# Optimization experiments

Hardware: AMD Instinct MI355X
Metric: run time of the kernel (lower is better)

## Reference

```python
import jax, jax.numpy as jnp
import numpy as np

N = 20000   # genes
E = 160000  # directed edges (self-loops added in forward, as PyG GATv2Conv does by default)
D = 64      # input feature dim
H1, C1 = 8, 128  # conv1 heads / channels
LRELU_SLOPE = 0.2
LN_EPS = 1e-5


def setup_inputs() -> dict:
    key = jax.random.key(0)
    ks = jax.random.split(key, 20)
    s = 0.05
    inp = {
        "x": jax.random.normal(ks[0], (N, D), dtype=jnp.float32),
        "edge_index": jax.random.randint(ks[1], (2, E), 0, N, dtype=jnp.int64),
        # conv1 (GATv2Conv D -> H1*C1, concat)
        "Wl1": jax.random.normal(ks[2], (D, H1 * C1), dtype=jnp.float32) * s,
        "bl1": jax.random.normal(ks[3], (H1 * C1,), dtype=jnp.float32) * s,
        "Wr1": jax.random.normal(ks[4], (D, H1 * C1), dtype=jnp.float32) * s,
        "br1": jax.random.normal(ks[5], (H1 * C1,), dtype=jnp.float32) * s,
        "att1": jax.random.normal(ks[6], (H1, C1), dtype=jnp.float32) * s,
        "b1": jax.random.normal(ks[7], (H1 * C1,), dtype=jnp.float32) * s,
        # skip Linear(D -> H1*C1)
        "Wskip": jax.random.normal(ks[8], (D, H1 * C1), dtype=jnp.float32) * s,
        "bskip": jax.random.normal(ks[9], (H1 * C1,), dtype=jnp.float32) * s,
        # LayerNorm(H1*C1)
        "g1": jnp.ones((H1 * C1,), dtype=jnp.float32),
        "beta1": jnp.zeros((H1 * C1,), dtype=jnp.float32),
        # conv2 (GATv2Conv H1*C1 -> 2, heads=1, concat=False)
        "Wl2": jax.random.normal(ks[10], (H1 * C1, 2), dtype=jnp.float32) * s,
        "bl2": jax.random.normal(ks[11], (2,), dtype=jnp.float32) * s,
        "Wr2": jax.random.normal(ks[12], (H1 * C1, 2), dtype=jnp.float32) * s,
        "br2": jax.random.normal(ks[13], (2,), dtype=jnp.float32) * s,
        "att2": jax.random.normal(ks[14], (1, 2), dtype=jnp.float32) * s,
        "b2": jax.random.normal(ks[15], (2,), dtype=jnp.float32) * s,
    }
    return inp


def _gatv2(x, src, dst, Wl, bl, Wr, br, att, bias, heads, ch, concat):
    """PyG GATv2Conv (eval mode): message src -> dst, scatter-softmax over dst."""
    n = x.shape[0]
    xl = (x @ Wl + bl).reshape(n, heads, ch)  # source-side transform
    xr = (x @ Wr + br).reshape(n, heads, ch)  # target-side transform
    e = jax.nn.leaky_relu(xl[src] + xr[dst], LRELU_SLOPE)   # [E,H,C]
    alpha = jnp.einsum('ehc,hc->eh', e, att)                 # [E,H]
    amax = jax.ops.segment_max(alpha, dst, num_segments=n)   # [N,H]
    ex = jnp.exp(alpha - amax[dst])
    denom = jax.ops.segment_sum(ex, dst, num_segments=n)
    alpha = ex / (denom[dst] + 1e-16)
    msg = xl[src] * alpha[..., None]                          # [E,H,C]
    out = jax.ops.segment_sum(msg, dst, num_segments=n)      # [N,H,C]
    out = out.reshape(n, heads * ch) if concat else out.mean(axis=1)
    return out + bias


def _layernorm(x, g, b):
    mu = x.mean(axis=-1, keepdims=True)
    var = ((x - mu) ** 2).mean(axis=-1, keepdims=True)
    return (x - mu) * jax.lax.rsqrt(var + LN_EPS) * g + b


def reference(x, edge_index, Wl1, bl1, Wr1, br1, att1, b1, Wskip, bskip,
              g1, beta1, Wl2, bl2, Wr2, br2, att2, b2):
    n = x.shape[0]
    loop = jnp.arange(n, dtype=edge_index.dtype)  # add_self_loops=True (PyG default)
    src = jnp.concatenate([edge_index[0], loop])
    dst = jnp.concatenate([edge_index[1], loop])
    x1 = _gatv2(x, src, dst, Wl1, bl1, Wr1, br1, att1, b1, H1, C1, True) + (x @ Wskip + bskip)
    x1 = jax.nn.elu(_layernorm(x1, g1, beta1))
    # dropout is a no-op in eval mode
    return _gatv2(x1, src, dst, Wl2, bl2, Wr2, br2, att2, b2, 1, 2, False)
```

## Files before the change

kernel.cpp:

```cpp
#include <hip/hip_runtime.h>
#include <hip/hip_bf16.h>
#include <hip/hip_fp16.h>
#include <math.h>

static constexpr int D  = 64;
static constexpr int F1 = 1024;
static constexpr int NTOT = 3072;
static constexpr int EW  = 64;

typedef _Float16 f16x8 __attribute__((ext_vector_type(8)));
typedef _Float16 h2    __attribute__((ext_vector_type(2)));
typedef float    f32x4 __attribute__((ext_vector_type(4)));
typedef unsigned int u32x4 __attribute__((ext_vector_type(4)));

__device__ __forceinline__ float lrelu(float x) { return x > 0.f ? x : 0.2f * x; }

__device__ __forceinline__ float dot2f(h2 a, h2 b, float c) {
#if __has_builtin(__builtin_amdgcn_fdot2)
    return __builtin_amdgcn_fdot2(a, b, c, false);
#else
    return c + (float)a[0] * (float)b[0] + (float)a[1] * (float)b[1];
#endif
}

__device__ __forceinline__ float red16(float p) {
    int v = __builtin_bit_cast(int, p);
    p += __builtin_bit_cast(float, __builtin_amdgcn_mov_dpp(v, 0xB1, 0xF, 0xF, true));
    v = __builtin_bit_cast(int, p);
    p += __builtin_bit_cast(float, __builtin_amdgcn_mov_dpp(v, 0x4E, 0xF, 0xF, true));
    v = __builtin_bit_cast(int, p);
    p += __builtin_bit_cast(float, __builtin_amdgcn_mov_dpp(v, 0x141, 0xF, 0xF, true));
    v = __builtin_bit_cast(int, p);
    p += __builtin_bit_cast(float, __builtin_amdgcn_mov_dpp(v, 0x140, 0xF, 0xF, true));
    return p;
}

union U4H { uint4 u; h2 h[4]; };

__global__ __launch_bounds__(256) void k_prep(
    const float* __restrict__ x, _Float16* __restrict__ xh,
    const int* __restrict__ ei, int* __restrict__ cursor,
    int* __restrict__ ell_off,
    const float* __restrict__ Wl1, const float* __restrict__ Wr1,
    const float* __restrict__ Wsk, _Float16* __restrict__ WhT,
    int n, int ne, int m, int castB, int degB)
{
    __shared__ _Float16 wt[128 * 72];
    const int b = blockIdx.x;
    if (b < castB) {
        int t = b * 256 + threadIdx.x;
        int ncast = (n * D) / 4;
        if (t < ncast) {
            float4 v = ((const float4*)x)[t];
            union { _Float16 h[4]; uint2 u; } o;
            o.h[0] = (_Float16)v.x; o.h[1] = (_Float16)v.y;
            o.h[2] = (_Float16)v.z; o.h[3] = (_Float16)v.w;
            *(uint2*)(xh + (size_t)t * 4) = o.u;
        }
    } else if (b < castB + degB) {
        int t = (b - castB) * 256 + threadIdx.x;
        if (t < m) {
            int s, d;
            if (t < ne) { s = ei[t]; d = ei[ne + t]; }
            else        { s = t - ne; d = s; }
            int c = atomicAdd(&cursor[d], 1);
            if (c < EW) ell_off[(d << 6) + c] = s << 11;
        }
    } else {
        const int t = threadIdx.x;
        const int c0 = (b - castB - degB) * 128;
        const float* __restrict__ W = (c0 < 1024) ? Wl1 : (c0 < 2048) ? Wr1 : Wsk;
        const int cw = c0 & 1023;
#pragma unroll
        for (int q = 0; q < 8; ++q) {
            int idx = t + 256 * q;
            int k = idx >> 5, c4 = (idx & 31) * 4;
            float4 v = *(const float4*)(W + (size_t)k * F1 + cw + c4);
            wt[(c4 + 0) * 72 + k] = (_Float16)v.x;
            wt[(c4 + 1) * 72 + k] = (_Float16)v.y;
            wt[(c4 + 2) * 72 + k] = (_Float16)v.z;
            wt[(c4 + 3) * 72 + k] = (_Float16)v.w;
        }
        __syncthreads();
#pragma unroll
        for (int q = 0; q < 4; ++q) {
            int idx = t + 256 * q;
            int c = idx >> 3, k0 = (idx & 7) * 8;
            uint4 v = *(const uint4*)(&wt[c * 72 + k0]);
            *(uint4*)(WhT + (size_t)(c0 + c) * 64 + k0) = v;
        }
    }
}

#define AS(r, c) smem[(r) * 72 + (c)]
#define BS(r, c) smem[128 * 72 + (r) * 72 + (c)]
#define CS(r, c) smem[(r) * 136 + (c)]
__global__ __launch_bounds__(256) void k_gemm_mfma(
    const _Float16* __restrict__ xh, const _Float16* __restrict__ WhT,
    const float* __restrict__ bl1, const float* __restrict__ br1,
    const float* __restrict__ bsk, const float* __restrict__ b1,
    _Float16* __restrict__ xl1h, _Float16* __restrict__ xr1h,
    _Float16* __restrict__ sk1h, int n)
{
    extern __shared__ _Float16 smem[];
    const int t  = threadIdx.x;
    const int r0 = blockIdx.x * 128;
    const int c0 = blockIdx.y * 128;

#pragma unroll
    for (int q = 0; q < 4; ++q) {
        int c = t + 256 * q;
        int row = c >> 3, off = (c & 7) * 8;
        uint4 v = make_uint4(0, 0, 0, 0);
        if (r0 + row < n) v = *(const uint4*)(xh + (size_t)(r0 + row) * 64 + off);
        *(uint4*)(&AS(row, off)) = v;
        uint4 w = *(const uint4*)(WhT + (size_t)(c0 + row) * 64 + off);
        *(uint4*)(&BS(row, off)) = w;
    }
    __syncthreads();

    const int wave = t >> 6, lane = t & 63;
    const int quad = lane >> 4, l16 = lane & 15;
    const int mw = (wave & 1) * 64, nw = (wave >> 1) * 64;

    f16x8 bfrag[4][2];
#pragma unroll
    for (int nt = 0; nt < 4; ++nt)
#pragma unroll
        for (int ks = 0; ks < 2; ++ks)
            bfrag[nt][ks] = *(const f16x8*)(&BS(nw + nt * 16 + l16, ks * 32 + quad * 8));

    f32x4 acc[4][4];
#pragma unroll
    for (int mt = 0; mt < 4; ++mt)
#pragma unroll
        for (int nt = 0; nt < 4; ++nt) acc[mt][nt] = (f32x4){0.f, 0.f, 0.f, 0.f};

#pragma unroll
    for (int mt = 0; mt < 4; ++mt) {
        f16x8 af[2];
#pragma unroll
        for (int ks = 0; ks < 2; ++ks)
            af[ks] = *(const f16x8*)(&AS(mw + mt * 16 + l16, ks * 32 + quad * 8));
#pragma unroll
        for (int nt = 0; nt < 4; ++nt)
#pragma unroll
            for (int ks = 0; ks < 2; ++ks)
                acc[mt][nt] = __builtin_amdgcn_mfma_f32_16x16x32_f16(
                    af[ks], bfrag[nt][ks], acc[mt][nt], 0, 0, 0);
    }

    const int which = c0 >> 10;
    const int csec  = c0 & 1023;
    __syncthreads();
#pragma unroll
    for (int nt = 0; nt < 4; ++nt) {
        int col = csec + nw + nt * 16 + l16;
        float bias = (which == 0) ? bl1[col] : (which == 1) ? br1[col]
                                             : (bsk[col] + b1[col]);
#pragma unroll
        for (int mt = 0; mt < 4; ++mt) {
#pragma unroll
            for (int r = 0; r < 4; ++r)
                CS(mw + mt * 16 + quad * 4 + r, nw + nt * 16 + l16) =
                    (_Float16)(acc[mt][nt][r] + bias);
        }
    }
    __syncthreads();

    _Float16* __restrict__ dst = (which == 0) ? xl1h : (which == 1) ? xr1h : sk1h;
#pragma unroll
    for (int it = 0; it < 8; ++it) {
        int idx = t + 256 * it;
        int row = idx >> 4, c16 = idx & 15;
        int grow = r0 + row;
        if (grow < n) {
            u32x4 v = *(u32x4*)(&CS(row, c16 * 8));
            *(u32x4*)(dst + (size_t)grow * F1 + csec + c16 * 8) = v;
        }
    }
}

__global__ __launch_bounds__(128, 6) void k_conv1_ln(
    const int* __restrict__ cursor, const int* __restrict__ ell_off,
    const _Float16* __restrict__ xl1h, const _Float16* __restrict__ xr1h,
    const _Float16* __restrict__ sk1h,
    const float* __restrict__ att1,
    const float* __restrict__ g1, const float* __restrict__ beta1,
    const float* __restrict__ Wl2, const float* __restrict__ bl2,
    const float* __restrict__ Wr2, const float* __restrict__ br2,
    float* __restrict__ xl2, float* __restrict__ xr2, int n)
{
    __shared__ float sb[2][6];
    const int q    = threadIdx.x >> 6;
    const int lane = threadIdx.x & 63;
    const int node = blockIdx.x;
    const int cb  = q * 512 + lane * 8;
    const int cbB = cb * 2;
    const h2 c02 = (h2){(_Float16)0.2f, (_Float16)0.2f};
    const char* __restrict__ xlB = (const char*)xl1h;

    int offv = ell_off[(node << 6) + lane];
    int deg  = cursor[node];
    deg = deg > EW ? EW : deg;

    h2 xrv[4], at2[4], O[4];
    float ll = 0.f;
    float v[8];
    float s1 = 0.f, s2 = 0.f;

    {
        U4H u; u.u = *(const uint4*)(xr1h + (size_t)node * F1 + cb);
#pragma unroll
        for (int j = 0; j < 4; ++j) xrv[j] = u.h[j];
        float4 a0 = *(const float4*)(att1 + cb);
        float4 a1 = *(const float4*)(att1 + cb + 4);
        at2[0] = (h2){(_Float16)a0.x, (_Float16)a0.y};
        at2[1] = (h2){(_Float16)a0.z, (_Float16)a0.w};
        at2[2] = (h2){(_Float16)a1.x, (_Float16)a1.y};
        at2[3] = (h2){(_Float16)a1.z, (_Float16)a1.w};
#pragma unroll
        for (int j = 0; j < 4; ++j) O[j] = (h2){(_Float16)0.f, (_Float16)0.f};
    }

    auto edge = [&](const U4H& cur) {
        h2 s0 = cur.h[0] + xrv[0];
        h2 s1h = cur.h[1] + xrv[1];
        h2 s2h = cur.h[2] + xrv[2];
        h2 s3 = cur.h[3] + xrv[3];
        h2 r0 = __builtin_elementwise_max(s0, s0 * c02);
        h2 r1 = __builtin_elementwise_max(s1h, s1h * c02);
        h2 r2 = __builtin_elementwise_max(s2h, s2h * c02);
        h2 r3 = __builtin_elementwise_max(s3, s3 * c02);
        float pa = dot2f(r0, at2[0], 0.f);
        float pb = dot2f(r1, at2[1], 0.f);
        pa = dot2f(r2, at2[2], pa);
        pb = dot2f(r3, at2[3], pb);
        float p = red16(pa + pb);
        float w = __expf(p);
        ll += w;
        _Float16 wh = (_Float16)w;
        h2 wh2 = (h2){wh, wh};
#pragma unroll
        for (int j = 0; j < 4; ++j) O[j] = O[j] + wh2 * cur.h[j];
    };

    auto ld = [&](int k) -> U4H {
        int kk = k < deg ? k : deg - 1;
        int off = __builtin_amdgcn_readlane(offv, kk);
        U4H u2; u2.u = *(const uint4*)(xlB + (unsigned)off + cbB);
        return u2;
    };
    {
        U4H A0 = ld(0), A1 = ld(1), A2 = ld(2), A3 = ld(3);
        U4H B0, B1, B2, B3, C0, C1, C2, C3;
        if (deg > 4) { B0 = ld(4); B1 = ld(5); B2 = ld(6); B3 = ld(7); }
        if (deg > 8) { C0 = ld(8); C1 = ld(9); C2 = ld(10); C3 = ld(11); }
        int i = 0;
        for (;;) {
            edge(A0);
            if (i + 1 < deg) edge(A1);
            if (i + 2 < deg) edge(A2);
            if (i + 3 < deg) edge(A3);
            i += 4;
            if (i >= deg) break;
            if (i + 8 < deg) { A0 = ld(i + 8); A1 = ld(i + 9);
                               A2 = ld(i + 10); A3 = ld(i + 11); }
            edge(B0);
            if (i + 1 < deg) edge(B1);
            if (i + 2 < deg) edge(B2);
            if (i + 3 < deg) edge(B3);
            i += 4;
            if (i >= deg) break;
            if (i + 8 < deg) { B0 = ld(i + 8); B1 = ld(i + 9);
                               B2 = ld(i + 10); B3 = ld(i + 11); }
            edge(C0);
            if (i + 1 < deg) edge(C1);
            if (i + 2 < deg) edge(C2);
            if (i + 3 < deg) edge(C3);
            i += 4;
            if (i >= deg) break;
            if (i + 8 < deg) { C0 = ld(i + 8); C1 = ld(i + 9);
                               C2 = ld(i + 10); C3 = ld(i + 11); }
        }
    }

    {
        float inv = 1.f / (ll + 1e-16f);
        U4H su; su.u = *(const uint4*)(sk1h + (size_t)node * F1 + cb);
#pragma unroll
        for (int j = 0; j < 4; ++j) {
            float xv0 = (float)su.h[j][0] + (float)O[j][0] * inv;
            float xv1 = (float)su.h[j][1] + (float)O[j][1] * inv;
            v[2 * j]     = xv0;
            v[2 * j + 1] = xv1;
            s1 += xv0 + xv1;
            s2 += xv0 * xv0 + xv1 * xv1;
        }
    }
#pragma unroll
    for (int off = 32; off > 0; off >>= 1) {
        s1 += __shfl_xor(s1, off);
        s2 += __shfl_xor(s2, off);
    }
    if (lane == 0) { sb[q][0] = s1; sb[q][1] = s2; }
    __syncthreads();
    float mu  = (sb[0][0] + sb[1][0]) * (1.f / 1024.f);
    float ms  = (sb[0][1] + sb[1][1]) * (1.f / 1024.f);
    float var = fmaxf(ms - mu * mu, 0.f);
    float inv = rsqrtf(var + 1e-5f);

    float p0 = 0.f, p1 = 0.f, p2 = 0.f, p3 = 0.f;
    {
        float4 gA = *(const float4*)(g1 + cb),    gB = *(const float4*)(g1 + cb + 4);
        float4 bA = *(const float4*)(beta1 + cb), bB = *(const float4*)(beta1 + cb + 4);
        float gv[8] = {gA.x, gA.y, gA.z, gA.w, gB.x, gB.y, gB.z, gB.w};
        float bv[8] = {bA.x, bA.y, bA.z, bA.w, bB.x, bB.y, bB.z, bB.w};
#pragma unroll
        for (int j = 0; j < 8; j += 2) {
            float4 wl = *(const float4*)(Wl2 + (cb + j) * 2);
            float4 wr = *(const float4*)(Wr2 + (cb + j) * 2);
            float y0 = (v[j]   - mu) * inv * gv[j]   + bv[j];
            float y1 = (v[j+1] - mu) * inv * gv[j+1] + bv[j+1];
            float z0 = y0 > 0.f ? y0 : __expf(y0) - 1.f;
            float z1 = y1 > 0.f ? y1 : __expf(y1) - 1.f;
            p0 += z0 * wl.x + z1 * wl.z;
            p1 += z0 * wl.y + z1 * wl.w;
            p2 += z0 * wr.x + z1 * wr.z;
            p3 += z0 * wr.y + z1 * wr.w;
        }
    }
#pragma unroll
    for (int off = 32; off > 0; off >>= 1) {
        p0 += __shfl_xor(p0, off); p1 += __shfl_xor(p1, off);
        p2 += __shfl_xor(p2, off); p3 += __shfl_xor(p3, off);
    }
    if (lane == 0) { sb[q][2] = p0; sb[q][3] = p1;
                     sb[q][4] = p2; sb[q][5] = p3; }
    __syncthreads();
    if (lane == 0 && q == 0) {
        *(float2*)(xl2 + 2 * node) =
            make_float2(sb[0][2] + sb[1][2] + bl2[0], sb[0][3] + sb[1][3] + bl2[1]);
        *(float2*)(xr2 + 2 * node) =
            make_float2(sb[0][4] + sb[1][4] + br2[0], sb[0][5] + sb[1][5] + br2[1]);
    }
}

__global__ __launch_bounds__(64) void k_conv2(
    const int* __restrict__ cursor, const int* __restrict__ ell_off,
    const float* __restrict__ xl2, const float* __restrict__ xr2,
    const float* __restrict__ att2, const float* __restrict__ b2,
    float* __restrict__ out2, int n)
{
    int d = blockIdx.x * blockDim.x + threadIdx.x;
    if (d >= n) return;
    float2 xr = *(const float2*)(xr2 + 2 * d);
    float a0w = att2[0], a1w = att2[1];
    float m = -INFINITY, l = 0.f, o0 = 0.f, o1 = 0.f;
    const int base = d << 6;
    int deg = cursor[d]; deg = deg > EW ? EW : deg;
    float2 pf[2];
    pf[0] = *(const float2*)(xl2 + (ell_off[base] >> 10));
    pf[1] = (1 < deg) ? *(const float2*)(xl2 + (ell_off[base + 1] >> 10)) : pf[0];
    for (int i = 0; i < deg; ++i) {
        float2 cur = pf[0];
        pf[0] = pf[1];
        if (i + 2 < deg) pf[1] = *(const float2*)(xl2 + (ell_off[base + i + 2] >> 10));
        float p = lrelu(cur.x + xr.x) * a0w + lrelu(cur.y + xr.y) * a1w;
        float nm = fmaxf(m, p);
        float sc = __expf(m - nm);
        float w  = __expf(p - nm);
        l = l * sc + w;
        o0 = o0 * sc + w * cur.x;
        o1 = o1 * sc + w * cur.y;
        m = nm;
    }
    float inv = 1.f / (l + 1e-16f);
    out2[2 * d + 0] = o0 * inv + b2[0];
    out2[2 * d + 1] = o1 * inv + b2[1];
}

extern "C" void kernel_launch(void* const* d_in, const int* in_sizes, int n_in,
                              void* d_out, int out_size, void* d_ws, size_t ws_size,
                              hipStream_t stream)
{
    const float* x     = (const float*)d_in[0];
    const int*   ei    = (const int*)  d_in[1];
    const float* Wl1   = (const float*)d_in[2];
    const float* bl1   = (const float*)d_in[3];
    const float* Wr1   = (const float*)d_in[4];
    const float* br1   = (const float*)d_in[5];
    const float* att1  = (const float*)d_in[6];
    const float* b1    = (const float*)d_in[7];
    const float* Wsk   = (const float*)d_in[8];
    const float* bsk   = (const float*)d_in[9];
    const float* g1    = (const float*)d_in[10];
    const float* beta1 = (const float*)d_in[11];
    const float* Wl2   = (const float*)d_in[12];
    const float* bl2   = (const float*)d_in[13];
    const float* Wr2   = (const float*)d_in[14];
    const float* br2   = (const float*)d_in[15];
    const float* att2  = (const float*)d_in[16];
    const float* b2    = (const float*)d_in[17];

    const int n  = in_sizes[0] / D;
    const int ne = in_sizes[1] / 2;
    const int m  = ne + n;

    float* ws = (float*)d_ws;
    size_t o = 0;
    _Float16* xl1h = (_Float16*)(ws + o); o += (size_t)n * F1 / 2;
    _Float16* xr1h = (_Float16*)(ws + o); o += (size_t)n * F1 / 2;
    _Float16* sk1h = (_Float16*)(ws + o); o += (size_t)n * F1 / 2;
    _Float16* xh   = (_Float16*)(ws + o); o += (size_t)n * D / 2;
    _Float16* WhT  = (_Float16*)(ws + o); o += (size_t)NTOT * 64 / 2;
    float* xl2    = ws + o; o += (size_t)n * 2;
    float* xr2    = ws + o; o += (size_t)n * 2;
    int* cursor   = (int*)(ws + o); o += (size_t)n;
    int* ell_off  = (int*)(ws + o); o += (size_t)n * EW;
    float* out2   = (float*)d_out;

    (void)hipMemsetAsync(cursor, 0, (size_t)n * sizeof(int), stream);
    const int castB = ((n * D) / 4 + 255) / 256;
    const int degB  = (m + 255) / 256;
    k_prep<<<castB + degB + NTOT / 128, 256, 0, stream>>>(
        x, xh, ei, cursor, ell_off, Wl1, Wr1, Wsk, WhT, n, ne, m, castB, degB);

    dim3 gg((n + 127) / 128, NTOT / 128);
    k_gemm_mfma<<<gg, 256, 36864, stream>>>(xh, WhT, bl1, br1, bsk, b1,
                                            xl1h, xr1h, sk1h, n);

    k_conv1_ln<<<n, 128, 0, stream>>>(cursor, ell_off, xl1h, xr1h, sk1h,
                                      att1, g1, beta1, Wl2, bl2, Wr2, br2,
                                      xl2, xr2, n);

    k_conv2<<<(n + 63) / 64, 64, 0, stream>>>(cursor, ell_off, xl2, xr2, att2, b2, out2, n);
}
```

Before: 203.4 us.

## Fuse prep kernel into GEMM: convert fp32 inputs in-tile, build ELL in extra grid row

Removes the separate prep kernel. The GEMM now loads fp32 x and the weight slices directly, converting and transposing them to fp16 in shared memory. An extra row of GEMM blocks takes over the edge-bucketing atomics that fill the ELL adjacency. This drops one launch and the round trip of the fp16 staging buffers through memory. In exchange, every GEMM block redoes the fp32 weight conversion, and its transposed shared-memory stores may hit bank conflicts.

Measured after the change: 219.4 us. 1.08x slower.

```diff
diff --git a/kernel.cpp b/kernel.cpp
--- a/kernel.cpp
+++ b/kernel.cpp
@@ -37,85 +37,61 @@
 
 union U4H { uint4 u; h2 h[4]; };
 
-__global__ __launch_bounds__(256) void k_prep(
-    const float* __restrict__ x, _Float16* __restrict__ xh,
-    const int* __restrict__ ei, int* __restrict__ cursor,
-    int* __restrict__ ell_off,
-    const float* __restrict__ Wl1, const float* __restrict__ Wr1,
-    const float* __restrict__ Wsk, _Float16* __restrict__ WhT,
-    int n, int ne, int m, int castB, int degB)
-{
-    __shared__ _Float16 wt[128 * 72];
-    const int b = blockIdx.x;
-    if (b < castB) {
-        int t = b * 256 + threadIdx.x;
-        int ncast = (n * D) / 4;
-        if (t < ncast) {
-            float4 v = ((const float4*)x)[t];
-            union { _Float16 h[4]; uint2 u; } o;
-            o.h[0] = (_Float16)v.x; o.h[1] = (_Float16)v.y;
-            o.h[2] = (_Float16)v.z; o.h[3] = (_Float16)v.w;
-            *(uint2*)(xh + (size_t)t * 4) = o.u;
-        }
-    } else if (b < castB + degB) {
-        int t = (b - castB) * 256 + threadIdx.x;
-        if (t < m) {
-            int s, d;
-            if (t < ne) { s = ei[t]; d = ei[ne + t]; }
-            else        { s = t - ne; d = s; }
-            int c = atomicAdd(&cursor[d], 1);
-            if (c < EW) ell_off[(d << 6) + c] = s << 11;
-        }
-    } else {
-        const int t = threadIdx.x;
-        const int c0 = (b - castB - degB) * 128;
-        const float* __restrict__ W = (c0 < 1024) ? Wl1 : (c0 < 2048) ? Wr1 : Wsk;
-        const int cw = c0 & 1023;
-#pragma unroll
-        for (int q = 0; q < 8; ++q) {
-            int idx = t + 256 * q;
-            int k = idx >> 5, c4 = (idx & 31) * 4;
-            float4 v = *(const float4*)(W + (size_t)k * F1 + cw + c4);
-            wt[(c4 + 0) * 72 + k] = (_Float16)v.x;
-            wt[(c4 + 1) * 72 + k] = (_Float16)v.y;
-            wt[(c4 + 2) * 72 + k] = (_Float16)v.z;
-            wt[(c4 + 3) * 72 + k] = (_Float16)v.w;
-        }
-        __syncthreads();
-#pragma unroll
-        for (int q = 0; q < 4; ++q) {
-            int idx = t + 256 * q;
-            int c = idx >> 3, k0 = (idx & 7) * 8;
-            uint4 v = *(const uint4*)(&wt[c * 72 + k0]);
-            *(uint4*)(WhT + (size_t)(c0 + c) * 64 + k0) = v;
-        }
-    }
-}
-
 #define AS(r, c) smem[(r) * 72 + (c)]
 #define BS(r, c) smem[128 * 72 + (r) * 72 + (c)]
 #define CS(r, c) smem[(r) * 136 + (c)]
 __global__ __launch_bounds__(256) void k_gemm_mfma(
-    const _Float16* __restrict__ xh, const _Float16* __restrict__ WhT,
+    const float* __restrict__ x,
+    const float* __restrict__ Wl1, const float* __restrict__ Wr1,
+    const float* __restrict__ Wsk,
     const float* __restrict__ bl1, const float* __restrict__ br1,
     const float* __restrict__ bsk, const float* __restrict__ b1,
     _Float16* __restrict__ xl1h, _Float16* __restrict__ xr1h,
-    _Float16* __restrict__ sk1h, int n)
+    _Float16* __restrict__ sk1h,
+    const int* __restrict__ ei, int* __restrict__ cursor,
+    int* __restrict__ ell_off,
+    int n, int ne, int m)
 {
     extern __shared__ _Float16 smem[];
     const int t  = threadIdx.x;
+
+    if (blockIdx.y == gridDim.y - 1) {
+        const int stride = gridDim.x * 256;
+        for (int e = blockIdx.x * 256 + t; e < m; e += stride) {
+            int s, d;
+            if (e < ne) { s = ei[e]; d = ei[ne + e]; }
+            else        { s = e - ne; d = s; }
+            int c = atomicAdd(&cursor[d], 1);
+            if (c < EW) ell_off[(d << 6) + c] = s << 11;
+        }
+        return;
+    }
+
     const int r0 = blockIdx.x * 128;
     const int c0 = blockIdx.y * 128;
-
-#pragma unroll
-    for (int q = 0; q < 4; ++q) {
-        int c = t + 256 * q;
-        int row = c >> 3, off = (c & 7) * 8;
-        uint4 v = make_uint4(0, 0, 0, 0);
-        if (r0 + row < n) v = *(const uint4*)(xh + (size_t)(r0 + row) * 64 + off);
-        *(uint4*)(&AS(row, off)) = v;
-        uint4 w = *(const uint4*)(WhT + (size_t)(c0 + row) * 64 + off);
-        *(uint4*)(&BS(row, off)) = w;
+    const float* __restrict__ W = (c0 < 1024) ? Wl1 : (c0 < 2048) ? Wr1 : Wsk;
+    const int cw = c0 & 1023;
+
+#pragma unroll
+    for (int qq = 0; qq < 8; ++qq) {
+        int idx = t + 256 * qq;
+        int row = idx >> 4, k4 = (idx & 15) * 4;
+        float4 v = make_float4(0.f, 0.f, 0.f, 0.f);
+        if (r0 + row < n) v = *(const float4*)(x + (size_t)(r0 + row) * D + k4);
+        union { _Float16 h[4]; uint2 u; } o;
+        o.h[0] = (_Float16)v.x; o.h[1] = (_Float16)v.y;
+        o.h[2] = (_Float16)v.z; o.h[3] = (_Float16)v.w;
+        *(uint2*)(&AS(row, k4)) = o.u;
+    }
+#pragma unroll
+    for (int qq = 0; qq < 8; ++qq) {
+        int idx = t + 256 * qq;
+        int k = idx >> 5, c4 = (idx & 31) * 4;
+        float4 v = *(const float4*)(W + (size_t)k * F1 + cw + c4);
+        BS(c4 + 0, k) = (_Float16)v.x;
+        BS(c4 + 1, k) = (_Float16)v.y;
+        BS(c4 + 2, k) = (_Float16)v.z;
+        BS(c4 + 3, k) = (_Float16)v.w;
     }
     __syncthreads();
 
@@ -412,8 +388,6 @@
     _Float16* xl1h = (_Float16*)(ws + o); o += (size_t)n * F1 / 2;
     _Float16* xr1h = (_Float16*)(ws + o); o += (size_t)n * F1 / 2;
     _Float16* sk1h = (_Float16*)(ws + o); o += (size_t)n * F1 / 2;
-    _Float16* xh   = (_Float16*)(ws + o); o += (size_t)n * D / 2;
-    _Float16* WhT  = (_Float16*)(ws + o); o += (size_t)NTOT * 64 / 2;
     float* xl2    = ws + o; o += (size_t)n * 2;
     float* xr2    = ws + o; o += (size_t)n * 2;
     int* cursor   = (int*)(ws + o); o += (size_t)n;
@@ -421,14 +395,13 @@
     float* out2   = (float*)d_out;
 
     (void)hipMemsetAsync(cursor, 0, (size_t)n * sizeof(int), stream);
-    const int castB = ((n * D) / 4 + 255) / 256;
-    const int degB  = (m + 255) / 256;
-    k_prep<<<castB + degB + NTOT / 128, 256, 0, stream>>>(
-        x, xh, ei, cursor, ell_off, Wl1, Wr1, Wsk, WhT, n, ne, m, castB, degB);
-
-    dim3 gg((n + 127) / 128, NTOT / 128);
-    k_gemm_mfma<<<gg, 256, 36864, stream>>>(xh, WhT, bl1, br1, bsk, b1,
-                                            xl1h, xr1h, sk1h, n);
+
+    dim3 gg((n + 127) / 128, NTOT / 128 + 1);
+    k_gemm_mfma<<<gg, 256, 36864, stream>>>(x, Wl1, Wr1, Wsk,
+                                            bl1, br1, bsk, b1,
+                                            xl1h, xr1h, sk1h,
+                                            ei, cursor, ell_off,
+                                            n, ne, m);
 
     k_conv1_ln<<<n, 128, 0, stream>>>(cursor, ell_off, xl1h, xr1h, sk1h,
                                       att1, g1, beta1, Wl2, bl2, Wr2, br2,
```
